# Optimization experiments

Hardware: AMD Instinct MI355X
Metric: run time of the kernel (lower is better)

Reference implementation:

```python
import jax, jax.numpy as jnp
import numpy as np

E = 8            # n_expert
K = 2            # n_expert_per_token
C = 2048         # n_embd
I = 1408         # moe_intermediate_size
IS = I * 2       # shared expert intermediate (n_shared_expert=2)
B, T = 2, 2048


def setup_inputs() -> dict:
    key = jax.random.key(0)
    ks = jax.random.split(key, 9)
    s = 0.02
    return {
        "x": jax.random.normal(ks[0], (B, T, C), dtype=jnp.float32),
        "gate_w": jax.random.normal(ks[1], (E, C), dtype=jnp.float32) * s,
        # expert MLP weights, torch Linear convention (out_features, in_features)
        "w1": jax.random.normal(ks[2], (E, I, C), dtype=jnp.float32) * s,  # fc_1
        "w2": jax.random.normal(ks[3], (E, I, C), dtype=jnp.float32) * s,  # fc_2
        "w3": jax.random.normal(ks[4], (E, C, I), dtype=jnp.float32) * s,  # proj
        # shared expert
        "sw1": jax.random.normal(ks[5], (IS, C), dtype=jnp.float32) * s,
        "sw2": jax.random.normal(ks[6], (IS, C), dtype=jnp.float32) * s,
        "sw3": jax.random.normal(ks[7], (C, IS), dtype=jnp.float32) * s,
    }


def reference(x, gate_w, w1, w2, w3, sw1, sw2, sw3):
    Bq, Tq, Cq = x.shape
    xf = x.reshape(-1, Cq)  # [N, C], N = B*T

    # top-k routing: softmax in fp32, then top-k probs per token
    logits = xf @ gate_w.T                                   # [N, E]
    probs = jax.nn.softmax(logits.astype(jnp.float32), axis=-1)
    topk_p, topk_i = jax.lax.top_k(probs, K)                 # [N, K]
    # combine weights: comb[n, e] = sum_k topk_p[n,k] * (topk_i[n,k] == e)
    comb = (jax.nn.one_hot(topk_i, E, dtype=jnp.float32)
            * topk_p[..., None]).sum(axis=1).astype(x.dtype)  # [N, E]

    # per-expert gated-SiLU MLP (batched over experts via einsum)
    h1 = jnp.einsum('nc,eic->eni', xf, w1)                   # [E, N, I]
    h2 = jnp.einsum('nc,eic->eni', xf, w2)                   # [E, N, I]
    h = jax.nn.silu(h1) * h2
    eo = jnp.einsum('eni,eci->enc', h, w3)                   # [E, N, C]

    # weighted scatter-combine
    y = jnp.einsum('enc,ne->nc', eo, comb).reshape(Bq, Tq, Cq)

    # shared expert on the residual input
    sh = (jax.nn.silu(xf @ sw1.T) * (xf @ sw2.T)) @ sw3.T    # [N, C]
    return y + sh.reshape(Bq, Tq, Cq)
```

## Files before the change

### kernel.cpp

```cpp
#include <hip/hip_runtime.h>
#include <stdint.h>

#define N_TOK 4096
#define CDIM  2048
#define NEXP  8
#define IDIM  1408
#define ISDIM 2816
#define CAP   2048
#define ICAT  2816
#define SCAT  5632

typedef __attribute__((ext_vector_type(8))) short bf16x8;
typedef __attribute__((ext_vector_type(4))) float f32x4;

#define GLOAD16(gp, lp) __builtin_amdgcn_global_load_lds( \
    (const __attribute__((address_space(1))) void*)(gp),  \
    (__attribute__((address_space(3))) void*)(lp), 16, 0, 0)

__device__ __forceinline__ unsigned short f2bf(float f) {
  union { float f; unsigned u; } c; c.f = f;
  return (unsigned short)((c.u + 0x7FFFu + ((c.u >> 16) & 1u)) >> 16);
}
__device__ __forceinline__ float bf2f(unsigned short h) {
  union { unsigned u; float f; } c; c.u = (unsigned)h << 16;
  return c.f;
}

__device__ __forceinline__ int xcd_swizzle(int orig, int nwg) {
  int q = nwg >> 3, r = nwg & 7;
  int xcd = orig & 7, idx = orig >> 3;
  return (xcd < r ? xcd * (q + 1) : r * (q + 1) + (xcd - r) * q) + idx;
}

__global__ __launch_bounds__(256) void cvt_all(
    const float* __restrict__ x, const float* __restrict__ w1,
    const float* __restrict__ w2, const float* __restrict__ w3,
    const float* __restrict__ sw1, const float* __restrict__ sw2,
    const float* __restrict__ sw3,
    unsigned short* __restrict__ xb, unsigned short* __restrict__ wcat,
    unsigned short* __restrict__ w3b, unsigned short* __restrict__ swcat,
    unsigned short* __restrict__ sw3b) {
  const int b = blockIdx.x;
  const int t = threadIdx.x;
  const float* src;
  unsigned short* dst;
  if (b < 4096) {
    src = x + (size_t)b * 2048;  dst = xb + (size_t)b * 2048;
  } else if (b < 15360) {
    size_t o = (size_t)(b - 4096) * 2048;  src = w3 + o;  dst = w3b + o;
  } else if (b < 18176) {
    size_t o = (size_t)(b - 15360) * 2048; src = sw3 + o; dst = sw3b + o;
  } else if (b < 40704) {
    int g = b - 18176;
    int e = g / 2816, r = g - e * 2816;
    int dr;
    if (r < 1408) { src = w1 + ((size_t)e * 1408 + r) * 2048; dr = (r >> 7) * 256 + (r & 127); }
    else { int r2 = r - 1408; src = w2 + ((size_t)e * 1408 + r2) * 2048; dr = (r2 >> 7) * 256 + 128 + (r2 & 127); }
    dst = wcat + ((size_t)e * ICAT + dr) * 2048;
  } else {
    int g = b - 40704;
    int dr;
    if (g < 2816) {
      int zn = g >= 1408, rr = g - zn * 1408;
      src = sw1 + (size_t)g * 2048;
      dr = zn * 2816 + (rr >> 7) * 256 + (rr & 127);
    } else {
      int r = g - 2816;
      int zn = r >= 1408, rr = r - zn * 1408;
      src = sw2 + (size_t)r * 2048;
      dr = zn * 2816 + (rr >> 7) * 256 + 128 + (rr & 127);
    }
    dst = swcat + (size_t)dr * 2048;
  }
  size_t i = (size_t)t * 8;
  float4 v0 = *(const float4*)(src + i);
  float4 v1 = *(const float4*)(src + i + 4);
  bf16x8 o;
  o[0] = (short)f2bf(v0.x); o[1] = (short)f2bf(v0.y);
  o[2] = (short)f2bf(v0.z); o[3] = (short)f2bf(v0.w);
  o[4] = (short)f2bf(v1.x); o[5] = (short)f2bf(v1.y);
  o[6] = (short)f2bf(v1.z); o[7] = (short)f2bf(v1.w);
  *(bf16x8*)(dst + i) = o;
}

__global__ __launch_bounds__(64) void routing_kernel(
    const float* __restrict__ x, const float* __restrict__ gw,
    int* __restrict__ counts, int* __restrict__ list,
    int* __restrict__ slot_of, float* __restrict__ wts) {
  const int n = blockIdx.x;
  const int lane = threadIdx.x;
  const float* xr = x + (size_t)n * CDIM;
  float s[NEXP];
#pragma unroll
  for (int e = 0; e < NEXP; e++) s[e] = 0.f;
  for (int c = lane; c < CDIM; c += 64) {
    float xv = xr[c];
#pragma unroll
    for (int e = 0; e < NEXP; e++) s[e] += xv * gw[e * CDIM + c];
  }
#pragma unroll
  for (int e = 0; e < NEXP; e++) {
    float v = s[e];
    for (int o = 32; o > 0; o >>= 1) v += __shfl_down(v, o);
    s[e] = v;
  }
  if (lane == 0) {
    float mx = s[0];
#pragma unroll
    for (int e = 1; e < NEXP; e++) mx = fmaxf(mx, s[e]);
    float p[NEXP], sum = 0.f;
#pragma unroll
    for (int e = 0; e < NEXP; e++) { p[e] = __expf(s[e] - mx); sum += p[e]; }
    int i0 = 0;
#pragma unroll
    for (int e = 1; e < NEXP; e++) if (p[e] > p[i0]) i0 = e;
    int i1 = (i0 == 0) ? 1 : 0;
#pragma unroll
    for (int e = 0; e < NEXP; e++) if (e != i0 && p[e] > p[i1]) i1 = e;
    float inv = 1.f / sum;
    int s0 = atomicAdd(&counts[i0], 1);
    int s1 = atomicAdd(&counts[i1], 1);
    if (s0 < CAP) list[i0 * CAP + s0] = n; else s0 = 0;
    if (s1 < CAP) list[i1 * CAP + s1] = n; else s1 = 0;
    slot_of[n * 2]     = i0 * CAP + s0;
    slot_of[n * 2 + 1] = i1 * CAP + s1;
    wts[n * 2]     = p[i0] * inv;
    wts[n * 2 + 1] = p[i1] * inv;
  }
}

template <int PHASE>
__global__ __launch_bounds__(512) void moe_gemm(
    const unsigned short* __restrict__ xb,
    const unsigned short* __restrict__ swcat,
    const unsigned short* __restrict__ wcat,
    unsigned short* __restrict__ hs_out,
    unsigned short* __restrict__ he_out,
    const unsigned short* __restrict__ hs,
    const unsigned short* __restrict__ sw3b,
    const unsigned short* __restrict__ he,
    const unsigned short* __restrict__ w3b,
    float* __restrict__ ysf,
    unsigned short* __restrict__ eo,
    const int* __restrict__ list,
    const int* __restrict__ counts) {
  const int z = blockIdx.z;
  const unsigned short *A, *B;
  unsigned short* O = nullptr;
  float* Of = nullptr;
  int Ka, ldo;
  int cnt = 1 << 30;
  const int* lst = nullptr;
  int Mt, Nt;
  bool gath = false;
  if (PHASE == 1) {
    Mt = 8; Nt = 11; Ka = CDIM;
    if (z < 4) {
      int zm = z >> 1, zn = z & 1;
      A = xb + (size_t)zm * 2048 * CDIM;
      B = swcat + (size_t)zn * 2816 * CDIM;
      O = hs_out + (size_t)zm * 2048 * ISDIM + (size_t)zn * 1408;
      ldo = ISDIM;
    } else {
      int e = z - 4;
      cnt = counts[e]; if (cnt > CAP) cnt = CAP;
      lst = list + e * CAP;
      gath = true;
      A = xb;
      B = wcat + (size_t)e * ICAT * CDIM;
      O = he_out + (size_t)e * CAP * IDIM;
      ldo = IDIM;
    }
  } else {
    Mt = 8; Nt = 8;
    if (z < 2) {
      Ka = ISDIM;
      A = hs + (size_t)z * 2048 * ISDIM;
      B = sw3b;
      Of = ysf + (size_t)z * 2048 * CDIM;
      ldo = CDIM;
    } else {
      int e = z - 2;
      cnt = counts[e]; if (cnt > CAP) cnt = CAP;
      Ka = IDIM;
      A = he + (size_t)e * CAP * IDIM;
      B = w3b + (size_t)e * CDIM * IDIM;
      O = eo + (size_t)e * CAP * CDIM;
      ldo = CDIM;
    }
  }
  const int wg = xcd_swizzle(blockIdx.x, Mt * Nt);
  const int mt = wg % Mt, nt = wg / Mt;
  if (mt * 256 >= cnt) return;

  __shared__ __align__(16) char lds[2][2][2][16384];

  const int tid = threadIdx.x;
  const int srow = tid >> 2;
  const int c16  = (tid & 3) << 4;
  const int scol = c16 ^ (((srow >> 1) & 3) << 4);
  const char* aS[2];
  const char* bS[2];
#pragma unroll
  for (int j = 0; j < 2; j++) {
    int ar = mt * 256 + j * 128 + srow;
    if (PHASE == 1 && gath) ar = (ar < cnt) ? lst[ar] : lst[0];
    aS[j] = (const char*)A + (size_t)ar * Ka * 2 + scol;
    int br = nt * 256 + j * 128 + srow;
    bS[j] = (const char*)B + (size_t)br * Ka * 2 + scol;
  }
  auto stageA = [&](int buf, int kt, int h) {
    size_t kb = (size_t)kt * 128 + (size_t)(h << 6);
    char* aD = &lds[buf][0][h][0] + tid * 16;
    GLOAD16(aS[0] + kb, aD);
    GLOAD16(aS[1] + kb, aD + 8192);
  };
  auto stageB = [&](int buf, int kt, int h) {
    size_t kb = (size_t)kt * 128 + (size_t)(h << 6);
    char* bD = &lds[buf][1][h][0] + tid * 16;
    GLOAD16(bS[0] + kb, bD);
    GLOAD16(bS[1] + kb, bD + 8192);
  };

  const int lane = tid & 63, wid = tid >> 6;
  const int wr = wid >> 2, wc = wid & 3;
  const int lrow = lane & 15;
  const int klane = (lane >> 4) << 4;
  const int rsw = ((lrow >> 1) & 3) << 4;
  const int aOff = (wr * 128 + lrow) * 64 + (klane ^ rsw);
  const int bOff = (wc * 64 + lrow) * 64 + (klane ^ rsw);

  f32x4 acc[8][4];
#pragma unroll
  for (int mf = 0; mf < 8; mf++)
#pragma unroll
    for (int nf = 0; nf < 4; nf++) acc[mf][nf] = (f32x4){0.f, 0.f, 0.f, 0.f};

  stageA(0, 0, 0); stageB(0, 0, 0);
  stageA(0, 0, 1); stageB(0, 0, 1);
  stageA(1, 1, 0); stageB(1, 1, 0);
  asm volatile("s_waitcnt vmcnt(8)" ::: "memory");
  __builtin_amdgcn_s_barrier();

#define MFMA_Q(MB)                                                             \
  _Pragma("unroll")                                                            \
  for (int nf = 0; nf < 4; nf++)                                               \
    _Pragma("unroll")                                                          \
    for (int m = 0; m < 4; m++)                                                \
      acc[(MB) * 4 + m][nf] = __builtin_amdgcn_mfma_f32_16x16x32_bf16(         \
          aR[m], bR[nf], acc[(MB) * 4 + m][nf], 0, 0, 0);

  const int ntk = Ka >> 6;
  for (int t = 0; t < ntk; t++) {
    const int p = t & 1;
    const char* aK0 = &lds[p][0][0][0];
    const char* aK1 = &lds[p][0][1][0];
    const char* bK0 = &lds[p][1][0][0];
    const char* bK1 = &lds[p][1][1][0];
    bf16x8 aR[4], bR[4];
#pragma unroll
    for (int i = 0; i < 4; i++) aR[i] = *(const bf16x8*)(aK0 + aOff + i * 1024);
#pragma unroll
    for (int i = 0; i < 4; i++) bR[i] = *(const bf16x8*)(bK0 + bOff + i * 1024);
    if (t + 1 < ntk) stageA(p ^ 1, t + 1, 1);
    __builtin_amdgcn_s_barrier();
    asm volatile("s_waitcnt lgkmcnt(0)" ::: "memory");
    __builtin_amdgcn_s_setprio(1);
    MFMA_Q(0)
    __builtin_amdgcn_s_setprio(0);
    __builtin_amdgcn_s_barrier();
#pragma unroll
    for (int i = 0; i < 4; i++) aR[i] = *(const bf16x8*)(aK0 + aOff + (i + 4) * 1024);
    if (t + 1 < ntk) {
      stageB(p ^ 1, t + 1, 1);
      asm volatile("s_waitcnt vmcnt(8)" ::: "memory");
    } else {
      asm volatile("s_waitcnt vmcnt(0)" ::: "memory");
    }
    __builtin_amdgcn_s_barrier();
    asm volatile("s_waitcnt lgkmcnt(0)" ::: "memory");
    __builtin_amdgcn_s_setprio(1);
    MFMA_Q(1)
    __builtin_amdgcn_s_setprio(0);
    __builtin_amdgcn_s_barrier();
#pragma unroll
    for (int i = 0; i < 4; i++) aR[i] = *(const bf16x8*)(aK1 + aOff + i * 1024);
#pragma unroll
    for (int i = 0; i < 4; i++) bR[i] = *(const bf16x8*)(bK1 + bOff + i * 1024);
    if (t + 2 < ntk) stageA(p, t + 2, 0);
    __builtin_amdgcn_s_barrier();
    asm volatile("s_waitcnt lgkmcnt(0)" ::: "memory");
    __builtin_amdgcn_s_setprio(1);
    MFMA_Q(0)
    __builtin_amdgcn_s_setprio(0);
    __builtin_amdgcn_s_barrier();
#pragma unroll
    for (int i = 0; i < 4; i++) aR[i] = *(const bf16x8*)(aK1 + aOff + (i + 4) * 1024);
    if (t + 2 < ntk) {
      stageB(p, t + 2, 0);
      asm volatile("s_waitcnt vmcnt(8)" ::: "memory");
    } else if (t + 1 < ntk) {
      asm volatile("s_waitcnt vmcnt(4)" ::: "memory");
    }
    __builtin_amdgcn_s_barrier();
    asm volatile("s_waitcnt lgkmcnt(0)" ::: "memory");
    __builtin_amdgcn_s_setprio(1);
    MFMA_Q(1)
    __builtin_amdgcn_s_setprio(0);
    __builtin_amdgcn_s_barrier();
  }
#undef MFMA_Q

  const int r4 = (lane >> 4) * 4;
  if (PHASE == 1) {
    float* ldsF = (float*)&lds[0][0][0][0];
    const int rbase = wr * 128 + r4;
    if (wc >= 2) {
      const int cb = (wc - 2) * 64;
#pragma unroll
      for (int mf = 0; mf < 8; mf++)
#pragma unroll
        for (int nf = 0; nf < 4; nf++) {
          int cc = cb + nf * 16 + lrow;
#pragma unroll
          for (int r = 0; r < 4; r++) {
            int rr = rbase + mf * 16 + r;
            ldsF[rr * 128 + (cc ^ (((rr >> 2) & 1) << 4))] = acc[mf][nf][r];
          }
        }
    }
    __syncthreads();
    if (wc < 2) {
      const int cb = wc * 64;
#pragma unroll
      for (int mf = 0; mf < 8; mf++) {
        int row0 = mt * 256 + wr * 128 + mf * 16 + r4;
#pragma unroll
        for (int nf = 0; nf < 4; nf++) {
          int cc = cb + nf * 16 + lrow;
          int col = nt * 128 + cc;
#pragma unroll
          for (int r = 0; r < 4; r++) {
            int rr = rbase + mf * 16 + r;
            float z1 = acc[mf][nf][r];
            float z2 = ldsF[rr * 128 + (cc ^ (((rr >> 2) & 1) << 4))];
            float gv = z1 / (1.f + __expf(-z1)) * z2;
            O[(size_t)(row0 + r) * ldo + col] = f2bf(gv);
          }
        }
      }
    }
  } else {
    const int rowb = mt * 256 + wr * 128;
    const int colb = nt * 256 + wc * 64;
#pragma unroll
    for (int mf = 0; mf < 8; mf++) {
      int row0 = rowb + mf * 16 + r4;
#pragma unroll
      for (int nf = 0; nf < 4; nf++) {
        int col = colb + nf * 16 + lrow;
#pragma unroll
        for (int r = 0; r < 4; r++) {
          if (z < 2)
            Of[(size_t)(row0 + r) * ldo + col] = acc[mf][nf][r];
          else
            O[(size_t)(row0 + r) * ldo + col] = f2bf(acc[mf][nf][r]);
        }
      }
    }
  }
}

__global__ __launch_bounds__(256) void combine_kernel(
    float* __restrict__ y, const float* __restrict__ ysf,
    const unsigned short* __restrict__ eo,
    const int* __restrict__ slot_of, const float* __restrict__ wts) {
  int idx = blockIdx.x * 256 + threadIdx.x;
  int n = idx >> 9;
  int c = (idx & 511) * 4;
  float4 v = *(const float4*)(ysf + (size_t)n * CDIM + c);
#pragma unroll
  for (int k = 0; k < 2; k++) {
    int slot = slot_of[n * 2 + k];
    float w = wts[n * 2 + k];
    ushort4 h = *(const ushort4*)(eo + (size_t)slot * CDIM + c);
    v.x += w * bf2f(h.x);
    v.y += w * bf2f(h.y);
    v.z += w * bf2f(h.z);
    v.w += w * bf2f(h.w);
  }
  *(float4*)(y + (size_t)n * CDIM + c) = v;
}

extern "C" void kernel_launch(void* const* d_in, const int* in_sizes, int n_in,
                              void* d_out, int out_size, void* d_ws, size_t ws_size,
                              hipStream_t stream) {
  const float* x   = (const float*)d_in[0];
  const float* gw  = (const float*)d_in[1];
  const float* w1  = (const float*)d_in[2];
  const float* w2  = (const float*)d_in[3];
  const float* w3  = (const float*)d_in[4];
  const float* sw1 = (const float*)d_in[5];
  const float* sw2 = (const float*)d_in[6];
  const float* sw3 = (const float*)d_in[7];
  float* y = (float*)d_out;

  char* ws = (char*)d_ws;
  size_t off = 0;
  auto alloc = [&](size_t b) -> void* {
    void* p = ws + off;
    off += (b + 255) & ~(size_t)255;
    return p;
  };
  unsigned short* xb    = (unsigned short*)alloc((size_t)N_TOK * CDIM * 2);
  unsigned short* wcat  = (unsigned short*)alloc((size_t)NEXP * ICAT * CDIM * 2);
  unsigned short* w3b   = (unsigned short*)alloc((size_t)NEXP * CDIM * IDIM * 2);
  unsigned short* swcat = (unsigned short*)alloc((size_t)SCAT * CDIM * 2);
  unsigned short* sw3b  = (unsigned short*)alloc((size_t)CDIM * ISDIM * 2);
  unsigned short* hs    = (unsigned short*)alloc((size_t)N_TOK * ISDIM * 2);
  unsigned short* he    = (unsigned short*)alloc((size_t)NEXP * CAP * IDIM * 2);
  float*          ysf   = (float*)alloc((size_t)N_TOK * CDIM * 4);
  int*   counts  = (int*)alloc(NEXP * 4);
  int*   list    = (int*)alloc((size_t)NEXP * CAP * 4);
  int*   slot_of = (int*)alloc((size_t)N_TOK * 2 * 4);
  float* wtsb    = (float*)alloc((size_t)N_TOK * 2 * 4);
  unsigned short* eoB = wcat;

  hipMemsetAsync(counts, 0, NEXP * 4, stream);
  routing_kernel<<<N_TOK, 64, 0, stream>>>(x, gw, counts, list, slot_of, wtsb);

  cvt_all<<<46336, 256, 0, stream>>>(x, w1, w2, w3, sw1, sw2, sw3,
                                     xb, wcat, w3b, swcat, sw3b);

  moe_gemm<1><<<dim3(88, 1, 12), 512, 0, stream>>>(
      xb, swcat, wcat, hs, he, hs, sw3b, he, w3b, ysf, eoB, list, counts);

  moe_gemm<2><<<dim3(64, 1, 10), 512, 0, stream>>>(
      xb, swcat, wcat, hs, he, hs, sw3b, he, w3b, ysf, eoB, list, counts);

  combine_kernel<<<(N_TOK * (CDIM / 4)) / 256, 256, 0, stream>>>(y, ysf, eoB, slot_of, wtsb);
}
```

Measured before the change: 591.3 us.

## Fuse combine into second GEMM epilogue via atomic scatter-add into output

Removes the separate combine kernel and the intermediate fp32 shared-output and bf16 expert-output buffers. The second GEMM's epilogue now atomically adds the shared-expert result and the routing-weighted expert results directly into the zeroed output, using per-slot weights stored by routing. This trades a full read/write pass and a launch for a large number of scalar fp32 global atomics. It also adds a memset of the output and makes the summation order nondeterministic.

```diff
diff --git a/kernel.cpp b/kernel.cpp
--- a/kernel.cpp
+++ b/kernel.cpp
@@ -86,7 +86,7 @@
 __global__ __launch_bounds__(64) void routing_kernel(
     const float* __restrict__ x, const float* __restrict__ gw,
     int* __restrict__ counts, int* __restrict__ list,
-    int* __restrict__ slot_of, float* __restrict__ wts) {
+    float* __restrict__ wslot) {
   const int n = blockIdx.x;
   const int lane = threadIdx.x;
   const float* xr = x + (size_t)n * CDIM;
@@ -120,12 +120,8 @@
     float inv = 1.f / sum;
     int s0 = atomicAdd(&counts[i0], 1);
     int s1 = atomicAdd(&counts[i1], 1);
-    if (s0 < CAP) list[i0 * CAP + s0] = n; else s0 = 0;
-    if (s1 < CAP) list[i1 * CAP + s1] = n; else s1 = 0;
-    slot_of[n * 2]     = i0 * CAP + s0;
-    slot_of[n * 2 + 1] = i1 * CAP + s1;
-    wts[n * 2]     = p[i0] * inv;
-    wts[n * 2 + 1] = p[i1] * inv;
+    if (s0 < CAP) { list[i0 * CAP + s0] = n; wslot[i0 * CAP + s0] = p[i0] * inv; }
+    if (s1 < CAP) { list[i1 * CAP + s1] = n; wslot[i1 * CAP + s1] = p[i1] * inv; }
   }
 }
 
@@ -140,17 +136,18 @@
     const unsigned short* __restrict__ sw3b,
     const unsigned short* __restrict__ he,
     const unsigned short* __restrict__ w3b,
-    float* __restrict__ ysf,
-    unsigned short* __restrict__ eo,
+    float* __restrict__ yout,
+    const float* __restrict__ wslot,
     const int* __restrict__ list,
     const int* __restrict__ counts) {
   const int z = blockIdx.z;
   const unsigned short *A, *B;
   unsigned short* O = nullptr;
   float* Of = nullptr;
-  int Ka, ldo;
+  int Ka, ldo = CDIM;
   int cnt = 1 << 30;
   const int* lst = nullptr;
+  const float* wsl = nullptr;
   int Mt, Nt;
   bool gath = false;
   if (PHASE == 1) {
@@ -177,16 +174,15 @@
       Ka = ISDIM;
       A = hs + (size_t)z * 2048 * ISDIM;
       B = sw3b;
-      Of = ysf + (size_t)z * 2048 * CDIM;
-      ldo = CDIM;
+      Of = yout + (size_t)z * 2048 * CDIM;
     } else {
       int e = z - 2;
       cnt = counts[e]; if (cnt > CAP) cnt = CAP;
       Ka = IDIM;
       A = he + (size_t)e * CAP * IDIM;
       B = w3b + (size_t)e * CDIM * IDIM;
-      O = eo + (size_t)e * CAP * CDIM;
-      ldo = CDIM;
+      lst = list + e * CAP;
+      wsl = wslot + e * CAP;
     }
   }
   const int wg = xcd_swizzle(blockIdx.x, Mt * Nt);
@@ -353,43 +349,36 @@
   } else {
     const int rowb = mt * 256 + wr * 128;
     const int colb = nt * 256 + wc * 64;
-#pragma unroll
-    for (int mf = 0; mf < 8; mf++) {
-      int row0 = rowb + mf * 16 + r4;
-#pragma unroll
-      for (int nf = 0; nf < 4; nf++) {
-        int col = colb + nf * 16 + lrow;
+    if (z < 2) {
+#pragma unroll
+      for (int mf = 0; mf < 8; mf++) {
+        int row0 = rowb + mf * 16 + r4;
 #pragma unroll
         for (int r = 0; r < 4; r++) {
-          if (z < 2)
-            Of[(size_t)(row0 + r) * ldo + col] = acc[mf][nf][r];
-          else
-            O[(size_t)(row0 + r) * ldo + col] = f2bf(acc[mf][nf][r]);
+          float* yrow = Of + (size_t)(row0 + r) * CDIM;
+#pragma unroll
+          for (int nf = 0; nf < 4; nf++)
+            atomicAdd(yrow + colb + nf * 16 + lrow, acc[mf][nf][r]);
         }
       }
-    }
-  }
-}
-
-__global__ __launch_bounds__(256) void combine_kernel(
-    float* __restrict__ y, const float* __restrict__ ysf,
-    const unsigned short* __restrict__ eo,
-    const int* __restrict__ slot_of, const float* __restrict__ wts) {
-  int idx = blockIdx.x * 256 + threadIdx.x;
-  int n = idx >> 9;
-  int c = (idx & 511) * 4;
-  float4 v = *(const float4*)(ysf + (size_t)n * CDIM + c);
-#pragma unroll
-  for (int k = 0; k < 2; k++) {
-    int slot = slot_of[n * 2 + k];
-    float w = wts[n * 2 + k];
-    ushort4 h = *(const ushort4*)(eo + (size_t)slot * CDIM + c);
-    v.x += w * bf2f(h.x);
-    v.y += w * bf2f(h.y);
-    v.z += w * bf2f(h.z);
-    v.w += w * bf2f(h.w);
-  }
-  *(float4*)(y + (size_t)n * CDIM + c) = v;
+    } else {
+#pragma unroll
+      for (int mf = 0; mf < 8; mf++) {
+        int row0 = rowb + mf * 16 + r4;
+#pragma unroll
+        for (int r = 0; r < 4; r++) {
+          int s = row0 + r;
+          if (s >= cnt) continue;
+          int tok = lst[s];
+          float w = wsl[s];
+          float* yrow = yout + (size_t)tok * CDIM;
+#pragma unroll
+          for (int nf = 0; nf < 4; nf++)
+            atomicAdd(yrow + colb + nf * 16 + lrow, w * acc[mf][nf][r]);
+        }
+      }
+    }
+  }
 }
 
 extern "C" void kernel_launch(void* const* d_in, const int* in_sizes, int n_in,
@@ -419,24 +408,20 @@
   unsigned short* sw3b  = (unsigned short*)alloc((size_t)CDIM * ISDIM * 2);
   unsigned short* hs    = (unsigned short*)alloc((size_t)N_TOK * ISDIM * 2);
   unsigned short* he    = (unsigned short*)alloc((size_t)NEXP * CAP * IDIM * 2);
-  float*          ysf   = (float*)alloc((size_t)N_TOK * CDIM * 4);
   int*   counts  = (int*)alloc(NEXP * 4);
   int*   list    = (int*)alloc((size_t)NEXP * CAP * 4);
-  int*   slot_of = (int*)alloc((size_t)N_TOK * 2 * 4);
-  float* wtsb    = (float*)alloc((size_t)N_TOK * 2 * 4);
-  unsigned short* eoB = wcat;
+  float* wslot   = (float*)alloc((size_t)NEXP * CAP * 4);
 
   hipMemsetAsync(counts, 0, NEXP * 4, stream);
-  routing_kernel<<<N_TOK, 64, 0, stream>>>(x, gw, counts, list, slot_of, wtsb);
+  hipMemsetAsync(y, 0, (size_t)N_TOK * CDIM * 4, stream);
+  routing_kernel<<<N_TOK, 64, 0, stream>>>(x, gw, counts, list, wslot);
 
   cvt_all<<<46336, 256, 0, stream>>>(x, w1, w2, w3, sw1, sw2, sw3,
                                      xb, wcat, w3b, swcat, sw3b);
 
   moe_gemm<1><<<dim3(88, 1, 12), 512, 0, stream>>>(
-      xb, swcat, wcat, hs, he, hs, sw3b, he, w3b, ysf, eoB, list, counts);
+      xb, swcat, wcat, hs, he, hs, sw3b, he, w3b, y, wslot, list, counts);
 
   moe_gemm<2><<<dim3(64, 1, 10), 512, 0, stream>>>(
-      xb, swcat, wcat, hs, he, hs, sw3b, he, w3b, ysf, eoB, list, counts);
-
-  combine_kernel<<<(N_TOK * (CDIM / 4)) / 256, 256, 0, stream>>>(y, ysf, eoB, slot_of, wtsb);
-}
+      xb, swcat, wcat, hs, he, hs, sw3b, he, w3b, y, wslot, list, counts);
+}
```

New measurement: 616.0 us. +4.2%, slower.

## Overlap w3/sw3 bf16 conversion with phase-1 GEMM via extra grid slice

Applied to the files above, without the earlier changes.

Moves the fp32-to-bf16 conversion of w3 and the shared sw3 out of the standalone conversion kernel and into an extra z-slice of the phase-1 GEMM launch. That slice's 88 blocks grid-stride over the weights, so the conversion runs alongside the first GEMM instead of before it. The goal is to hide the memory-bound conversion under the compute-bound GEMM. In exchange, the converting blocks compete with the GEMM for bandwidth and CU slots, and they may be scheduled late in the launch, which would extend its tail.

```diff
diff --git a/kernel.cpp b/kernel.cpp
--- a/kernel.cpp
+++ b/kernel.cpp
@@ -34,31 +34,25 @@
 
 __global__ __launch_bounds__(256) void cvt_all(
     const float* __restrict__ x, const float* __restrict__ w1,
-    const float* __restrict__ w2, const float* __restrict__ w3,
+    const float* __restrict__ w2,
     const float* __restrict__ sw1, const float* __restrict__ sw2,
-    const float* __restrict__ sw3,
     unsigned short* __restrict__ xb, unsigned short* __restrict__ wcat,
-    unsigned short* __restrict__ w3b, unsigned short* __restrict__ swcat,
-    unsigned short* __restrict__ sw3b) {
+    unsigned short* __restrict__ swcat) {
   const int b = blockIdx.x;
   const int t = threadIdx.x;
   const float* src;
   unsigned short* dst;
   if (b < 4096) {
     src = x + (size_t)b * 2048;  dst = xb + (size_t)b * 2048;
-  } else if (b < 15360) {
-    size_t o = (size_t)(b - 4096) * 2048;  src = w3 + o;  dst = w3b + o;
-  } else if (b < 18176) {
-    size_t o = (size_t)(b - 15360) * 2048; src = sw3 + o; dst = sw3b + o;
-  } else if (b < 40704) {
-    int g = b - 18176;
+  } else if (b < 26624) {
+    int g = b - 4096;
     int e = g / 2816, r = g - e * 2816;
     int dr;
     if (r < 1408) { src = w1 + ((size_t)e * 1408 + r) * 2048; dr = (r >> 7) * 256 + (r & 127); }
     else { int r2 = r - 1408; src = w2 + ((size_t)e * 1408 + r2) * 2048; dr = (r2 >> 7) * 256 + 128 + (r2 & 127); }
     dst = wcat + ((size_t)e * ICAT + dr) * 2048;
   } else {
-    int g = b - 40704;
+    int g = b - 26624;
     int dr;
     if (g < 2816) {
       int zn = g >= 1408, rr = g - zn * 1408;
@@ -143,8 +137,32 @@
     float* __restrict__ ysf,
     unsigned short* __restrict__ eo,
     const int* __restrict__ list,
-    const int* __restrict__ counts) {
+    const int* __restrict__ counts,
+    const float* __restrict__ w3f,
+    const float* __restrict__ sw3f,
+    unsigned short* __restrict__ w3b_mut,
+    unsigned short* __restrict__ sw3b_mut) {
   const int z = blockIdx.z;
+  if (PHASE == 1 && z == 12) {
+    const size_t W3E  = (size_t)NEXP * CDIM * IDIM;
+    const size_t TOTE = W3E + (size_t)CDIM * ISDIM;
+    const size_t stride = (size_t)88 * 512 * 8;
+    for (size_t i = ((size_t)blockIdx.x * 512 + threadIdx.x) * 8; i < TOTE; i += stride) {
+      const float* s;
+      unsigned short* d;
+      if (i < W3E) { s = w3f + i; d = w3b_mut + i; }
+      else         { s = sw3f + (i - W3E); d = sw3b_mut + (i - W3E); }
+      float4 v0 = *(const float4*)s;
+      float4 v1 = *(const float4*)(s + 4);
+      bf16x8 o;
+      o[0] = (short)f2bf(v0.x); o[1] = (short)f2bf(v0.y);
+      o[2] = (short)f2bf(v0.z); o[3] = (short)f2bf(v0.w);
+      o[4] = (short)f2bf(v1.x); o[5] = (short)f2bf(v1.y);
+      o[6] = (short)f2bf(v1.z); o[7] = (short)f2bf(v1.w);
+      *(bf16x8*)d = o;
+    }
+    return;
+  }
   const unsigned short *A, *B;
   unsigned short* O = nullptr;
   float* Of = nullptr;
@@ -429,14 +447,15 @@
   hipMemsetAsync(counts, 0, NEXP * 4, stream);
   routing_kernel<<<N_TOK, 64, 0, stream>>>(x, gw, counts, list, slot_of, wtsb);
 
-  cvt_all<<<46336, 256, 0, stream>>>(x, w1, w2, w3, sw1, sw2, sw3,
-                                     xb, wcat, w3b, swcat, sw3b);
-
-  moe_gemm<1><<<dim3(88, 1, 12), 512, 0, stream>>>(
-      xb, swcat, wcat, hs, he, hs, sw3b, he, w3b, ysf, eoB, list, counts);
+  cvt_all<<<32256, 256, 0, stream>>>(x, w1, w2, sw1, sw2, xb, wcat, swcat);
+
+  moe_gemm<1><<<dim3(88, 1, 13), 512, 0, stream>>>(
+      xb, swcat, wcat, hs, he, hs, sw3b, he, w3b, ysf, eoB, list, counts,
+      w3, sw3, w3b, sw3b);
 
   moe_gemm<2><<<dim3(64, 1, 10), 512, 0, stream>>>(
-      xb, swcat, wcat, hs, he, hs, sw3b, he, w3b, ysf, eoB, list, counts);
+      xb, swcat, wcat, hs, he, hs, sw3b, he, w3b, ysf, eoB, list, counts,
+      nullptr, nullptr, nullptr, nullptr);
 
   combine_kernel<<<(N_TOK * (CDIM / 4)) / 256, 256, 0, stream>>>(y, ysf, eoB, slot_of, wtsb);
 }
```

New measurement: 570.0 us. 1.04x faster.
